# Kernel optimization log

Hardware: AMD Instinct MI355X
Metric: run time of the kernel (lower is better)

The kernel has to match this reference:

```python
import jax, jax.numpy as jnp
import numpy as np

ORIENTATIONS = 9
CELL = (8, 8)
BLOCK = (3, 3)
EPS = 1e-5  # skimage L2 block-norm epsilon


def _hog_features(x):
    # transform_sqrt=True (gamma compression)
    img = jnp.sqrt(x)
    H, W = img.shape
    # skimage _hog_channel_gradient: central differences, zero at borders
    g_row = jnp.zeros_like(img).at[1:-1, :].set(img[2:, :] - img[:-2, :])
    g_col = jnp.zeros_like(img).at[:, 1:-1].set(img[:, 2:] - img[:, :-2])
    mag = jnp.hypot(g_row, g_col)
    # orientation in degrees, folded to [0, 180)
    ori = jnp.rad2deg(jnp.arctan2(g_row, g_col)) % 180.0

    cr, cc = CELL
    ncr, ncc = H // cr, W // cc
    mag_c = mag[: ncr * cr, : ncc * cc]
    ori_c = ori[: ncr * cr, : ncc * cc]
    unit = 180.0 / ORIENTATIONS

    # hard binning (skimage uses no interpolation); small fixed loop over bins
    hists = []
    for b in range(ORIENTATIONS):
        sel = (ori_c >= b * unit) & (ori_c < (b + 1) * unit)
        m = jnp.where(sel, mag_c, 0.0)
        # per-cell mean of selected magnitudes: [ncr, ncc]
        cell = m.reshape(ncr, cr, ncc, cc).mean(axis=(1, 3))
        hists.append(cell)
    hist = jnp.stack(hists, axis=-1)  # [ncr, ncc, orientations]

    br_n, bc_n = BLOCK
    nbr, nbc = ncr - br_n + 1, ncc - bc_n + 1
    # overlapping blocks: [nbr, nbc, br_n, bc_n, orientations]
    blocks = jnp.stack(
        [jnp.stack([hist[i : i + nbr, j : j + nbc] for j in range(bc_n)], axis=2)
         for i in range(br_n)],
        axis=2,
    )
    # L2 block normalization: b / sqrt(sum(b^2) + eps^2)
    denom = jnp.sqrt(jnp.sum(blocks * blocks, axis=(2, 3, 4), keepdims=True) + EPS ** 2)
    normalized = blocks / denom
    return normalized.reshape(-1)  # feature_vector=True


def setup_inputs() -> dict:
    key = jax.random.key(0)
    x = jax.random.uniform(key, (4096, 4096), dtype=jnp.float32)
    return {"x": x}


def reference(x):
    return _hog_features(x)
```

## Files before the change

### kernel.cpp

```cpp
#include <hip/hip_runtime.h>
#include <math.h>

#define H 4096
#define W 4096
#define NC 512
#define NB 510
#define ORI 9
#define NCELLS (NC * NC)
#define NOUT (NB * NB * 81)

__device__ __forceinline__ float fdlibm_atanf(float x) {
#pragma clang fp contract(off)
    const float one = 1.0f;
    const float aT0  = (float) 3.33333333333329318027e-01;
    const float aT1  = (float)-1.99999999998764832476e-01;
    const float aT2  = (float) 1.42857142725034663711e-01;
    const float aT3  = (float)-1.11111104054623557880e-01;
    const float aT4  = (float) 9.09088713343650656196e-02;
    const float aT5  = (float)-7.69187620504482999495e-02;
    const float aT6  = (float) 6.66107313738753120669e-02;
    const float aT7  = (float)-5.83357013379057348645e-02;
    const float aT8  = (float) 4.97687799461593236017e-02;
    const float aT9  = (float)-3.65315727442169155270e-02;
    const float aT10 = (float) 1.62858201153657823623e-02;
    const float athi[4] = {4.6364760399e-01f, 7.8539812565e-01f,
                           9.8279368877e-01f, 1.5707962513e+00f};
    const float atlo[4] = {5.0121582440e-09f, 3.7748947079e-08f,
                           3.4473217170e-08f, 7.5497894159e-08f};
    int hx = __float_as_int(x);
    int ix = hx & 0x7fffffff;
    int id;
    if (ix >= 0x4c800000) {
        if (ix > 0x7f800000) return x + x;
        float r = athi[3] + atlo[3];
        return (hx > 0) ? r : -r;
    }
    if (ix < 0x3ee00000) {
        if (ix < 0x31000000) return x;
        id = -1;
    } else {
        x = fabsf(x);
        if (ix < 0x3f980000) {
            if (ix < 0x3f300000) { id = 0; x = (2.0f * x - one) / (2.0f + x); }
            else                 { id = 1; x = (x - one) / (x + one); }
        } else {
            if (ix < 0x401c0000) { id = 2; x = (x - 1.5f) / (one + 1.5f * x); }
            else                 { id = 3; x = -1.0f / x; }
        }
    }
    float z = x * x;
    float w = z * z;
    float s1 = z * (aT0 + w * (aT2 + w * (aT4 + w * (aT6 + w * (aT8 + w * aT10)))));
    float s2 = w * (aT1 + w * (aT3 + w * (aT5 + w * (aT7 + w * aT9))));
    if (id < 0) return x - x * (s1 + s2);
    z = athi[id] - ((x * (s1 + s2) - atlo[id]) - x);
    return (hx < 0) ? -z : z;
}

__device__ __forceinline__ float fdlibm_atan2f(float y, float x) {
#pragma clang fp contract(off)
    const float tiny   = 1.0e-30f;
    const float pi     = 3.1415927410e+00f;
    const float pi_lo  = -8.7422776573e-08f;
    const float pi_o_2 = 1.5707963705e+00f;
    int hx = __float_as_int(x), ix = hx & 0x7fffffff;
    int hy = __float_as_int(y), iy = hy & 0x7fffffff;
    if (hx == 0x3f800000) return fdlibm_atanf(y);
    int m = ((hy >> 31) & 1) | ((hx >> 30) & 2);
    if (iy == 0) {
        switch (m) {
            case 0: case 1: return y;
            case 2: return pi + tiny;
            default: return -pi - tiny;
        }
    }
    if (ix == 0) return (hy < 0) ? -pi_o_2 - tiny : pi_o_2 + tiny;
    int k = (iy - ix) >> 23;
    float z;
    if (k > 26) { z = pi_o_2 + 0.5f * pi_lo; m &= 1; }
    else if (k < -26 && hx < 0) z = 0.0f;
    else z = fdlibm_atanf(fabsf(y / x));
    switch (m) {
        case 0: return z;
        case 1: return -z;
        case 2: return pi - (z - pi_lo);
        default: return (z - pi_lo) - pi;
    }
}

__device__ __forceinline__ int slow_bin_px(const float* __restrict__ x,
                                           int grow, int gc,
                                           bool row_ok, bool col_ok) {
#pragma clang fp contract(off)
    float gy = 0.0f, gx = 0.0f;
    if (row_ok)
        gy = sqrtf(x[(grow + 1) * W + gc]) - sqrtf(x[(grow - 1) * W + gc]);
    if (col_ok)
        gx = sqrtf(x[grow * W + gc + 1]) - sqrtf(x[grow * W + gc - 1]);
    float ang = fdlibm_atan2f(gy, gx);
    const float RAD2DEG = (float)(180.0 / 3.14159265358979323846264338328);
    float deg = ang * RAD2DEG;
    float m = fmodf(deg, 180.0f);
    if (m < 0.0f) m += 180.0f;
    int bin = (int)(m / 20.0f);
    if (bin < 9 && m >= (float)((bin + 1) * 20)) bin++;
    else if (bin > 0 && m < (float)(bin * 20)) bin--;
    return bin;
}

#define T20 ((float) 0.36397023426620236135)
#define T40 ((float) 0.83909963117728001176)
#define T60 ((float) 1.73205080756887729353)
#define T80 ((float) 5.67128181961771110517)

__device__ __forceinline__ float f4c(const float4& v, int c) {
    switch (c) { case 0: return v.x; case 1: return v.y;
                 case 2: return v.z; default: return v.w; }
}

__global__ __launch_bounds__(256, 4) void hog_hist(const float* __restrict__ x,
                                                   float* __restrict__ hist,
                                                   float* __restrict__ q) {
    int t = threadIdx.x;
    int w = t >> 6, lane = t & 63;
    int wid = blockIdx.x * 4 + w;
    int crow = wid >> 4;
    int cs   = wid & 15;
    int gc0  = (cs << 8) + (lane << 2);

    int r0 = (crow << 3) - 1;
    int rtop = (r0 < 0) ? 0 : r0;
    int rbot = (r0 + 9 > H - 1) ? (H - 1) : (r0 + 9);
    int gcl = (gc0 == 0) ? 0 : gc0 - 1;
    int gcr = (gc0 + 4 > W - 1) ? (W - 1) : gc0 + 4;

    const float4* x4 = (const float4*)x;
    int c4 = (gc0 >> 2);
    float4 s4[10];
    s4[0] = x4[rtop * 1024 + c4];
#pragma unroll
    for (int k = 1; k < 9; ++k) s4[k] = x4[(r0 + k) * 1024 + c4];
    s4[9] = x4[rbot * 1024 + c4];
    float sL[8], sR[8];
#pragma unroll
    for (int j = 0; j < 8; ++j) {
        int grow = (crow << 3) + j;
        sL[j] = x[grow * W + gcl];
        sR[j] = x[grow * W + gcr];
    }
#pragma unroll
    for (int k = 0; k < 10; ++k) {
        s4[k].x = __builtin_amdgcn_sqrtf(s4[k].x);
        s4[k].y = __builtin_amdgcn_sqrtf(s4[k].y);
        s4[k].z = __builtin_amdgcn_sqrtf(s4[k].z);
        s4[k].w = __builtin_amdgcn_sqrtf(s4[k].w);
    }
#pragma unroll
    for (int j = 0; j < 8; ++j) {
        sL[j] = __builtin_amdgcn_sqrtf(sL[j]);
        sR[j] = __builtin_amdgcn_sqrtf(sR[j]);
    }

    bool okL = (gc0 >= 1);
    bool okR = (gc0 + 3 <= W - 2);
    float SA = 0.f, TA1 = 0.f, TA2 = 0.f, TA3 = 0.f, TA4 = 0.f;
    float SB = 0.f, TB1 = 0.f, TB2 = 0.f, TB3 = 0.f, TB4 = 0.f;
    unsigned gbits = 0;

#pragma unroll
    for (int j = 0; j < 8; ++j) {
        int grow = (crow << 3) + j;
        bool row_ok = (grow >= 1) && (grow <= H - 2);
#pragma unroll
        for (int c = 0; c < 4; ++c) {
            float gy = row_ok ? (f4c(s4[j + 2], c) - f4c(s4[j], c)) : 0.0f;
            float left  = (c == 0) ? sL[j] : f4c(s4[j + 1], c - 1);
            float right = (c == 3) ? sR[j] : f4c(s4[j + 1], c + 1);
            bool col_ok = (c == 0) ? okL : ((c == 3) ? okR : true);
            float gx = col_ok ? (right - left) : 0.0f;

            float a = fabsf(gy), b = fabsf(gx);
            float d1 = fmaf(b, -T20, a);
            float d2 = fmaf(b, -T40, a);
            float d3 = fmaf(b, -T60, a);
            float d4 = fmaf(b, -T80, a);
            float cm = fminf(fminf(fabsf(d1), fabsf(d2)),
                             fminf(fminf(fabsf(d3), fabsf(d4)), a));
            bool guard = cm < fmaf(1e-5f, a + b, 4e-6f);
            if (guard) gbits |= (1u << (j * 4 + c));

            bool opp = ((__float_as_int(gy) ^ __float_as_int(gx)) < 0);
            float mag = __builtin_amdgcn_sqrtf(fmaf(gy, gy, gx * gx));
            float magA = (!opp && !guard) ? mag : 0.0f;
            float magB = (opp && !guard) ? mag : 0.0f;

            SA  += magA;
            TA1 += (d1 > 0.0f) ? magA : 0.0f;
            TA2 += (d2 > 0.0f) ? magA : 0.0f;
            TA3 += (d3 > 0.0f) ? magA : 0.0f;
            TA4 += (d4 > 0.0f) ? magA : 0.0f;
            SB  += magB;
            TB1 += (d1 > 0.0f) ? magB : 0.0f;
            TB2 += (d2 > 0.0f) ? magB : 0.0f;
            TB3 += (d3 > 0.0f) ? magB : 0.0f;
            TB4 += (d4 > 0.0f) ? magB : 0.0f;
        }
    }

    float bb[9];
    bb[0] = SA - TA1;  bb[1] = TA1 - TA2;  bb[2] = TA2 - TA3;  bb[3] = TA3 - TA4;
    bb[4] = TA4 + TB4;
    bb[5] = TB3 - TB4; bb[6] = TB2 - TB3;  bb[7] = TB1 - TB2;  bb[8] = SB - TB1;

    if (__any(gbits != 0)) {
        unsigned gb = gbits;
        while (gb) {
            int bpos = __ffs(gb) - 1;
            gb &= gb - 1;
            int j = bpos >> 2, c = bpos & 3;
            int grow = (crow << 3) + j;
            int gc = gc0 + c;
            bool row_ok = (grow >= 1) && (grow <= H - 2);
            bool col_ok = (gc >= 1) && (gc <= W - 2);
            int bin = slow_bin_px(x, grow, gc, row_ok, col_ok);
            float gyE = 0.0f, gxE = 0.0f;
            if (row_ok) gyE = sqrtf(x[(grow + 1) * W + gc]) - sqrtf(x[(grow - 1) * W + gc]);
            if (col_ok) gxE = sqrtf(x[grow * W + gc + 1]) - sqrtf(x[grow * W + gc - 1]);
            float mag = sqrtf(fmaf(gyE, gyE, gxE * gxE));
#pragma unroll
            for (int b2 = 0; b2 < 9; ++b2) bb[b2] += (bin == b2) ? mag : 0.0f;
        }
    }

#pragma unroll
    for (int b2 = 0; b2 < 9; ++b2) {
        int tv = __builtin_amdgcn_update_dpp(0, __float_as_int(bb[b2]),
                                             0xB1, 0xF, 0xF, true);
        bb[b2] += __int_as_float(tv);
    }

    int cell = lane >> 1;
    int k = lane & 1;
    int cbase = crow * (NC * ORI) + ((cs << 5) + cell) * 9;
#pragma unroll
    for (int e = 0; e < 5; ++e) {
        float v0 = bb[e];
        float v1 = (e < 4) ? bb[5 + e] : 0.0f;
        float val = k ? v1 : v0;
        int off = k ? (5 + e) : e;
        if (!k || e < 4) hist[cbase + off] = val * (1.0f / 64.0f);
    }
    if (k == 0) {
        float qq = 0.0f;
#pragma unroll
        for (int b2 = 0; b2 < 9; ++b2) {
            float h = bb[b2] * (1.0f / 64.0f);
            qq = fmaf(h, h, qq);
        }
        q[crow * NC + (cs << 5) + cell] = qq;
    }
}

__global__ __launch_bounds__(256) void hog_inv(const float* __restrict__ q,
                                               float* __restrict__ inv) {
    int t = blockIdx.x * 256 + threadIdx.x;
    if (t >= NB * NB) return;
    int i = t / NB;
    int j = t - i * NB;
    float ssq = 0.0f;
#pragma unroll
    for (int bi = 0; bi < 3; ++bi)
#pragma unroll
        for (int bj = 0; bj < 3; ++bj)
            ssq += q[(i + bi) * NC + (j + bj)];
    inv[t] = 1.0f / sqrtf(ssq + 1e-10f);
}

__global__ __launch_bounds__(256) void hog_norm4(const float* __restrict__ hist,
                                                 const float* __restrict__ inv,
                                                 float4* __restrict__ out4, int n4) {
    int v = blockIdx.x * 256 + threadIdx.x;
    if (v >= n4) return;
    int k0 = v * 4;
    float r[4];
#pragma unroll
    for (int e = 0; e < 4; ++e) {
        int k = k0 + e;
        int pidx = k / 81;
        int e81 = k - pidx * 81;
        int i = pidx / NB;
        int j = pidx - i * NB;
        int bi = e81 / 27;
        int rr = e81 - bi * 27;
        int bj = rr / 9;
        int o = rr - bj * 9;
        r[e] = hist[((i + bi) * NC + (j + bj)) * ORI + o] * inv[pidx];
    }
    out4[v] = make_float4(r[0], r[1], r[2], r[3]);
}

extern "C" void kernel_launch(void* const* d_in, const int* in_sizes, int n_in,
                              void* d_out, int out_size, void* d_ws, size_t ws_size,
                              hipStream_t stream) {
    const float* x = (const float*)d_in[0];
    float* out = (float*)d_out;
    float* hist = (float*)d_ws;
    float* inv  = hist + NCELLS * ORI;
    float* q = out + (NOUT - NCELLS);

    hog_hist<<<(NC * 16) / 4, 256, 0, stream>>>(x, hist, q);
    hog_inv<<<(NB * NB + 255) / 256, 256, 0, stream>>>(q, inv);
    int n4 = out_size / 4;
    hog_norm4<<<(n4 + 255) / 256, 256, 0, stream>>>(hist, inv, (float4*)out, n4);
}
```

Measured before the change: 65.69 us.

## Split histogram row loop into two half passes and raise occupancy target

```diff
diff --git a/kernel.cpp b/kernel.cpp
--- a/kernel.cpp
+++ b/kernel.cpp
@@ -118,64 +118,54 @@
                  case 2: return v.z; default: return v.w; }
 }
 
-__global__ __launch_bounds__(256, 4) void hog_hist(const float* __restrict__ x,
-                                                   float* __restrict__ hist,
-                                                   float* __restrict__ q) {
-    int t = threadIdx.x;
-    int w = t >> 6, lane = t & 63;
-    int wid = blockIdx.x * 4 + w;
-    int crow = wid >> 4;
-    int cs   = wid & 15;
-    int gc0  = (cs << 8) + (lane << 2);
-
-    int r0 = (crow << 3) - 1;
-    int rtop = (r0 < 0) ? 0 : r0;
-    int rbot = (r0 + 9 > H - 1) ? (H - 1) : (r0 + 9);
-    int gcl = (gc0 == 0) ? 0 : gc0 - 1;
-    int gcr = (gc0 + 4 > W - 1) ? (W - 1) : gc0 + 4;
-
+__device__ __forceinline__ void hist_pass(const float* __restrict__ x, int crow,
+                                          int gc0, int jb, int gcl, int gcr,
+                                          bool okL, bool okR,
+                                          float& SA, float& TA1, float& TA2,
+                                          float& TA3, float& TA4,
+                                          float& SB, float& TB1, float& TB2,
+                                          float& TB3, float& TB4,
+                                          unsigned& gbits) {
+    int r0p = (crow << 3) + jb - 1;
+    int rtop = (r0p < 0) ? 0 : r0p;
+    int rbot = (r0p + 5 > H - 1) ? (H - 1) : (r0p + 5);
     const float4* x4 = (const float4*)x;
-    int c4 = (gc0 >> 2);
-    float4 s4[10];
+    int c4 = gc0 >> 2;
+
+    float4 s4[6];
     s4[0] = x4[rtop * 1024 + c4];
 #pragma unroll
-    for (int k = 1; k < 9; ++k) s4[k] = x4[(r0 + k) * 1024 + c4];
-    s4[9] = x4[rbot * 1024 + c4];
-    float sL[8], sR[8];
-#pragma unroll
-    for (int j = 0; j < 8; ++j) {
-        int grow = (crow << 3) + j;
-        sL[j] = x[grow * W + gcl];
-        sR[j] = x[grow * W + gcr];
-    }
-#pragma unroll
-    for (int k = 0; k < 10; ++k) {
+    for (int k = 1; k < 5; ++k) s4[k] = x4[(r0p + k) * 1024 + c4];
+    s4[5] = x4[rbot * 1024 + c4];
+    float sL[4], sR[4];
+#pragma unroll
+    for (int jr = 0; jr < 4; ++jr) {
+        int grow = (crow << 3) + jb + jr;
+        sL[jr] = x[grow * W + gcl];
+        sR[jr] = x[grow * W + gcr];
+    }
+#pragma unroll
+    for (int k = 0; k < 6; ++k) {
         s4[k].x = __builtin_amdgcn_sqrtf(s4[k].x);
         s4[k].y = __builtin_amdgcn_sqrtf(s4[k].y);
         s4[k].z = __builtin_amdgcn_sqrtf(s4[k].z);
         s4[k].w = __builtin_amdgcn_sqrtf(s4[k].w);
     }
 #pragma unroll
-    for (int j = 0; j < 8; ++j) {
-        sL[j] = __builtin_amdgcn_sqrtf(sL[j]);
-        sR[j] = __builtin_amdgcn_sqrtf(sR[j]);
-    }
-
-    bool okL = (gc0 >= 1);
-    bool okR = (gc0 + 3 <= W - 2);
-    float SA = 0.f, TA1 = 0.f, TA2 = 0.f, TA3 = 0.f, TA4 = 0.f;
-    float SB = 0.f, TB1 = 0.f, TB2 = 0.f, TB3 = 0.f, TB4 = 0.f;
-    unsigned gbits = 0;
-
-#pragma unroll
-    for (int j = 0; j < 8; ++j) {
-        int grow = (crow << 3) + j;
+    for (int jr = 0; jr < 4; ++jr) {
+        sL[jr] = __builtin_amdgcn_sqrtf(sL[jr]);
+        sR[jr] = __builtin_amdgcn_sqrtf(sR[jr]);
+    }
+
+#pragma unroll
+    for (int jr = 0; jr < 4; ++jr) {
+        int grow = (crow << 3) + jb + jr;
         bool row_ok = (grow >= 1) && (grow <= H - 2);
 #pragma unroll
         for (int c = 0; c < 4; ++c) {
-            float gy = row_ok ? (f4c(s4[j + 2], c) - f4c(s4[j], c)) : 0.0f;
-            float left  = (c == 0) ? sL[j] : f4c(s4[j + 1], c - 1);
-            float right = (c == 3) ? sR[j] : f4c(s4[j + 1], c + 1);
+            float gy = row_ok ? (f4c(s4[jr + 2], c) - f4c(s4[jr], c)) : 0.0f;
+            float left  = (c == 0) ? sL[jr] : f4c(s4[jr + 1], c - 1);
+            float right = (c == 3) ? sR[jr] : f4c(s4[jr + 1], c + 1);
             bool col_ok = (c == 0) ? okL : ((c == 3) ? okR : true);
             float gx = col_ok ? (right - left) : 0.0f;
 
@@ -187,7 +177,7 @@
             float cm = fminf(fminf(fabsf(d1), fabsf(d2)),
                              fminf(fminf(fabsf(d3), fabsf(d4)), a));
             bool guard = cm < fmaf(1e-5f, a + b, 4e-6f);
-            if (guard) gbits |= (1u << (j * 4 + c));
+            if (guard) gbits |= (1u << ((jb + jr) * 4 + c));
 
             bool opp = ((__float_as_int(gy) ^ __float_as_int(gx)) < 0);
             float mag = __builtin_amdgcn_sqrtf(fmaf(gy, gy, gx * gx));
@@ -206,6 +196,31 @@
             TB4 += (d4 > 0.0f) ? magB : 0.0f;
         }
     }
+}
+
+__global__ __launch_bounds__(256, 8) void hog_hist(const float* __restrict__ x,
+                                                   float* __restrict__ hist,
+                                                   float* __restrict__ q) {
+    int t = threadIdx.x;
+    int lane = t & 63;
+    int wid = blockIdx.x * 4 + (t >> 6);
+    int crow = wid >> 4;
+    int cs   = wid & 15;
+    int gc0  = (cs << 8) + (lane << 2);
+
+    int gcl = (gc0 == 0) ? 0 : gc0 - 1;
+    int gcr = (gc0 + 4 > W - 1) ? (W - 1) : gc0 + 4;
+    bool okL = (gc0 >= 1);
+    bool okR = (gc0 + 3 <= W - 2);
+
+    float SA = 0.f, TA1 = 0.f, TA2 = 0.f, TA3 = 0.f, TA4 = 0.f;
+    float SB = 0.f, TB1 = 0.f, TB2 = 0.f, TB3 = 0.f, TB4 = 0.f;
+    unsigned gbits = 0;
+
+    hist_pass(x, crow, gc0, 0, gcl, gcr, okL, okR,
+              SA, TA1, TA2, TA3, TA4, SB, TB1, TB2, TB3, TB4, gbits);
+    hist_pass(x, crow, gc0, 4, gcl, gcr, okL, okR,
+              SA, TA1, TA2, TA3, TA4, SB, TB1, TB2, TB3, TB4, gbits);
 
     float bb[9];
     bb[0] = SA - TA1;  bb[1] = TA1 - TA2;  bb[2] = TA2 - TA3;  bb[3] = TA3 - TA4;
```

Measured after the change: 67.65 us. +3.0%, slower.
